# Kernel tuning notes

Hardware: AMD Instinct MI355X
Metric: run time of the kernel (lower is better)

## Reference

```python
import jax, jax.numpy as jnp
import numpy as np

EPS_CLAMP = 1.0 - 1e-06


def _patch_pool_view(x, H, W, p):
    # x: (n, H*W, s) with spatial flattened row-major over (H, W)
    # -> (n, (H//p)*(W//p), p*p, s), matching einops 'n (h ph w pw) s -> n (h w) (ph pw) s'
    n, q, s = x.shape
    h, w = H // p, W // p
    x = x.reshape(n, h, p, w, p, s)
    x = x.transpose(0, 1, 3, 2, 4, 5)  # n h w ph pw s
    return x.reshape(n, h * w, p * p, s)


def setup_inputs() -> dict:
    key = jax.random.key(0)
    k1, k2 = jax.random.split(key)
    N, C, H, W = 8, 256, 48, 48
    return {
        'mask_feats': jax.random.normal(k1, (N, C, H, W), dtype=jnp.float32),
        'query_feats_all': jax.random.normal(k2, (N, C, H, W), dtype=jnp.float32),
        'path_size': 4,
    }


def reference(mask_feats, query_feats_all, path_size):
    N, c_m, hm, wm = mask_feats.shape
    _, c_q, hq, wq = query_feats_all.shape
    # n c h w -> n (h w) c, scaled by 1/sqrt(c)
    mf = mask_feats.reshape(N, c_m, hm * wm).transpose(0, 2, 1) / (c_m ** 0.5)
    qf = query_feats_all.reshape(N, c_q, hq * wq).transpose(0, 2, 1) / (c_q ** 0.5)
    sim_matrix = jnp.einsum('nqc,nsc->nqs', qf, mf) * 10.0  # (N, Q, S)
    instance_masks = jax.nn.softmax(sim_matrix, axis=1)
    query_masks = jnp.swapaxes(jax.nn.softmax(sim_matrix, axis=2), 1, 2)  # (N, S, Q)
    # patch pooling (computed under torch.no_grad in original)
    tmp_instance_masks_d = jax.lax.stop_gradient(
        _patch_pool_view(instance_masks, hq, wq, path_size))
    instance_masks_d = jnp.minimum(tmp_instance_masks_d.sum(axis=2), EPS_CLAMP)
    tmp_query_masks_d = jax.lax.stop_gradient(
        _patch_pool_view(query_masks, hm, wm, path_size))
    query_masks_d = jnp.minimum(tmp_query_masks_d.sum(axis=2), EPS_CLAMP)
    return (instance_masks, query_masks, instance_masks_d, query_masks_d,
            tmp_instance_masks_d, tmp_query_masks_d)
```

## Files before the change

kernel.cpp:

```cpp
#include <hip/hip_runtime.h>
#include <hip/hip_bf16.h>

#define N_B 8
#define CH 256
#define HW 2304
#define SZ_QS (2304LL*2304LL)
#define SCALE 0.0390625f
#define EPSC 0.999999f

typedef __attribute__((ext_vector_type(8))) short bf8_t;
typedef __attribute__((ext_vector_type(4))) float f32x4;

#define O1 0LL
#define O2 42467328LL
#define O3 84934656LL
#define O4 87588864LL
#define O5 90243072LL
#define O6 132710400LL

__device__ __forceinline__ void gl_lds16(const unsigned short* g, unsigned short* l) {
  __builtin_amdgcn_global_load_lds(
      (const __attribute__((address_space(1))) unsigned int*)g,
      (__attribute__((address_space(3))) unsigned int*)l, 16, 0, 0);
}

__global__ __launch_bounds__(256) void k_tr(const float* __restrict__ q_in,
                                            const float* __restrict__ m_in,
                                            __hip_bfloat16* __restrict__ Abf,
                                            __hip_bfloat16* __restrict__ Bbf) {
  __shared__ float lds[64 * 65];
  const int n = blockIdx.z >> 1, which = blockIdx.z & 1;
  const float* src = which ? m_in : q_in;
  __hip_bfloat16* dst = which ? Bbf : Abf;
  const int q0 = blockIdx.x * 64, c0 = blockIdx.y * 64;
  const int tx = threadIdx.x & 63, ty = threadIdx.x >> 6;
#pragma unroll
  for (int p = 0; p < 16; ++p) {
    const int cl = p * 4 + ty;
    lds[cl * 65 + tx] = src[((size_t)n * CH + c0 + cl) * HW + q0 + tx];
  }
  __syncthreads();
#pragma unroll
  for (int p = 0; p < 16; ++p) {
    const int ql = p * 4 + ty;
    dst[((size_t)n * HW + q0 + ql) * CH + c0 + tx] = __float2bfloat16(lds[tx * 65 + ql]);
  }
}

__global__ __launch_bounds__(256) void k_zero(float* __restrict__ p) {
  const int i = (blockIdx.x * 256 + threadIdx.x) * 4;
  *(float4*)(p + i) = make_float4(0.f, 0.f, 0.f, 0.f);
}

__global__ __launch_bounds__(256) void k_inv(const float* __restrict__ s,
                                             float* __restrict__ inv) {
  const int i = blockIdx.x * 256 + threadIdx.x;
  inv[i] = 1.0f / s[i];
}

template <int FULL>
__global__ __launch_bounds__(512) void k_g192(
    const unsigned short* __restrict__ Abf, const unsigned short* __restrict__ Bbf,
    float* __restrict__ out1, float* __restrict__ out2, float* __restrict__ out3,
    float* __restrict__ out4, float* __restrict__ out5, float* __restrict__ out6,
    float* __restrict__ rowsum, float* __restrict__ colsum,
    const float* __restrict__ invr, const float* __restrict__ invc) {
  __shared__ char smem[49152];
  unsigned short* lA = (unsigned short*)smem;
  unsigned short* lB = (unsigned short*)(smem + 24576);

  const int n = blockIdx.z;
  const int S0 = blockIdx.x * 192, Q0 = blockIdx.y * 192;
  const int t = threadIdx.x, l = t & 63, w = t >> 6;
  const int wm = w >> 2, wn = w & 3;
  const int g = l >> 4, c = l & 15;

  f32x4 acc[6][3];
#pragma unroll
  for (int mi = 0; mi < 6; ++mi)
#pragma unroll
    for (int ni = 0; ni < 3; ++ni) {
      f32x4 z = {0.f, 0.f, 0.f, 0.f};
      acc[mi][ni] = z;
    }

  const int r0w = w * 24;
  const int lrow = l >> 3, lc8 = l & 7;
  const int scol = (lc8 ^ lrow) * 8;
  const unsigned short* gA = Abf + ((size_t)n * HW + Q0 + r0w + lrow) * CH + scol;
  const unsigned short* gB = Bbf + ((size_t)n * HW + S0 + r0w + lrow) * CH + scol;
  unsigned short* dA = lA + r0w * 64;
  unsigned short* dB = lB + r0w * 64;

  for (int kc = 0; kc < 4; ++kc) {
    const int k0 = kc * 64;
    gl_lds16(gA + k0, dA);
    gl_lds16(gA + k0 + 8 * CH, dA + 8 * 64);
    gl_lds16(gA + k0 + 16 * CH, dA + 16 * 64);
    gl_lds16(gB + k0, dB);
    gl_lds16(gB + k0 + 8 * CH, dB + 8 * 64);
    gl_lds16(gB + k0 + 16 * CH, dB + 16 * 64);
    __syncthreads();
#pragma unroll
    for (int ks = 0; ks < 2; ++ks) {
      const int kb = ks * 4 + g;
      bf8_t af[6], bf_[3];
#pragma unroll
      for (int mi = 0; mi < 6; ++mi) {
        const int r = wm * 96 + mi * 16 + c;
        af[mi] = *(const bf8_t*)(lA + r * 64 + ((kb ^ (c & 7)) * 8));
      }
#pragma unroll
      for (int ni = 0; ni < 3; ++ni) {
        const int r = wn * 48 + ni * 16 + c;
        bf_[ni] = *(const bf8_t*)(lB + r * 64 + ((kb ^ (c & 7)) * 8));
      }
#pragma unroll
      for (int mi = 0; mi < 6; ++mi)
#pragma unroll
        for (int ni = 0; ni < 3; ++ni)
          acc[mi][ni] = __builtin_amdgcn_mfma_f32_16x16x32_bf16(af[mi], bf_[ni], acc[mi][ni], 0, 0, 0);
    }
    __syncthreads();
  }

#pragma unroll
  for (int mi = 0; mi < 6; ++mi)
#pragma unroll
    for (int ni = 0; ni < 3; ++ni)
#pragma unroll
      for (int r = 0; r < 4; ++r)
        acc[mi][ni][r] = __expf(acc[mi][ni][r] * SCALE);

  if (!FULL) {
#pragma unroll
    for (int mi = 0; mi < 6; ++mi)
#pragma unroll
      for (int r = 0; r < 4; ++r) {
        float v = acc[mi][0][r] + acc[mi][1][r] + acc[mi][2][r];
        v += __shfl_xor(v, 1, 64);
        v += __shfl_xor(v, 2, 64);
        v += __shfl_xor(v, 4, 64);
        v += __shfl_xor(v, 8, 64);
        if (c == 0) atomicAdd(&rowsum[n * HW + Q0 + wm * 96 + mi * 16 + g * 4 + r], v);
      }
#pragma unroll
    for (int ni = 0; ni < 3; ++ni) {
      float v = 0.f;
#pragma unroll
      for (int mi = 0; mi < 6; ++mi)
#pragma unroll
        for (int r = 0; r < 4; ++r) v += acc[mi][ni][r];
      v += __shfl_xor(v, 16, 64);
      v += __shfl_xor(v, 32, 64);
      if (g == 0) atomicAdd(&colsum[n * HW + S0 + wn * 48 + ni * 16 + c], v);
    }
    return;
  }

  float icv[3];
#pragma unroll
  for (int ni = 0; ni < 3; ++ni) icv[ni] = invc[n * HW + S0 + wn * 48 + ni * 16 + c];

  float* fb = (float*)smem;
  const int hq = blockIdx.y, bx = blockIdx.x;

#pragma unroll
  for (int ch = 0; ch < 4; ++ch) {
    if (wm == (ch >> 1)) {
#pragma unroll
      for (int m3 = 0; m3 < 3; ++m3) {
        const int mi = (ch & 1) * 3 + m3;
        const int rowb = m3 * 16 + g * 4;
#pragma unroll
        for (int ni = 0; ni < 3; ++ni) {
          const int colb = wn * 48 + ni * 16 + c;
#pragma unroll
          for (int r = 0; r < 4; ++r)
            fb[(rowb + r) * 196 + colb] = acc[mi][ni][r] * icv[ni];
        }
      }
    }
    __syncthreads();
#pragma unroll
    for (int j = 0; j < 5; ++j) {
      const int idx = t + j * 512;
      if (idx < 2304) {
        const int row = idx / 48, col4 = idx % 48;
        const float4 v = *(const float4*)(fb + row * 196 + col4 * 4);
        *(float4*)(out1 + ((size_t)n * HW + Q0 + ch * 48 + row) * HW + S0 + col4 * 4) = v;
        const size_t r5 = ((size_t)n * 144 + hq * 12 + (row >> 2)) * 16 + ch * 4 + (row & 3);
        *(float4*)(out5 + r5 * HW + S0 + col4 * 4) = v;
      }
    }
    __syncthreads();
  }

#pragma unroll
  for (int ch = 0; ch < 4; ++ch) {
    if (wn == ch) {
#pragma unroll
      for (int mi = 0; mi < 6; ++mi) {
        const int colf = wm * 96 + mi * 16 + g * 4;
        const f32x4 irv = *(const f32x4*)(invr + n * HW + Q0 + colf);
#pragma unroll
        for (int ni = 0; ni < 3; ++ni) {
          const f32x4 pq = acc[mi][ni] * irv;
          *(f32x4*)(fb + (ni * 16 + c) * 196 + colf) = pq;
        }
      }
    }
    __syncthreads();
#pragma unroll
    for (int j = 0; j < 5; ++j) {
      const int idx = t + j * 512;
      if (idx < 2304) {
        const int row = idx / 48, col4 = idx % 48;
        const float4 v = *(const float4*)(fb + row * 196 + col4 * 4);
        *(float4*)(out2 + ((size_t)n * HW + S0 + ch * 48 + row) * HW + Q0 + col4 * 4) = v;
        const size_t r6 = ((size_t)n * 144 + bx * 12 + (row >> 2)) * 16 + ch * 4 + (row & 3);
        *(float4*)(out6 + r6 * HW + Q0 + col4 * 4) = v;
      }
    }
    __syncthreads();
  }

#pragma unroll
  for (int m3 = 0; m3 < 3; ++m3) {
    const int b = m3 * 4 + g;
#pragma unroll
    for (int ni = 0; ni < 3; ++ni) {
      const int sl = wn * 48 + ni * 16 + c;
      float p = 0.f;
#pragma unroll
      for (int r = 0; r < 4; ++r) p += acc[m3][ni][r] + acc[m3 + 3][ni][r];
      fb[(wm * 12 + b) * 196 + sl] = p * icv[ni];
    }
  }
  __syncthreads();
#pragma unroll
  for (int j = 0; j < 5; ++j) {
    const int idx = t + j * 512;
    if (idx < 2304) {
      const int b = idx / 192, sl = idx % 192;
      const float v = fb[b * 196 + sl] + fb[(12 + b) * 196 + sl];
      out3[((size_t)n * 144 + hq * 12 + b) * HW + S0 + sl] = fminf(v, EPSC);
    }
  }
  __syncthreads();

#pragma unroll
  for (int mi = 0; mi < 6; ++mi) {
    const int qloc = wm * 96 + mi * 16 + g * 4;
    const f32x4 irv = *(const f32x4*)(invr + n * HW + Q0 + qloc);
#pragma unroll
    for (int ni = 0; ni < 3; ++ni) {
      f32x4 pq = acc[mi][ni] * irv;
#pragma unroll
      for (int r = 0; r < 4; ++r) {
        pq[r] += __shfl_xor(pq[r], 1, 64);
        pq[r] += __shfl_xor(pq[r], 2, 64);
      }
      if ((c & 3) == 0) {
        const int pc = ni * 4 + (c >> 2);
        *(f32x4*)(fb + (wn * 12 + pc) * 196 + qloc) = pq;
      }
    }
  }
  __syncthreads();
#pragma unroll
  for (int j = 0; j < 5; ++j) {
    const int idx = t + j * 512;
    if (idx < 2304) {
      const int pc = idx / 192, q = idx % 192;
      const float v = fb[pc * 196 + q] + fb[(12 + pc) * 196 + q] +
                      fb[(24 + pc) * 196 + q] + fb[(36 + pc) * 196 + q];
      out4[((size_t)n * 144 + bx * 12 + pc) * HW + Q0 + q] = fminf(v, EPSC);
    }
  }
}

__global__ __launch_bounds__(256) void k_gemm_old(const unsigned short* __restrict__ Abf,
                                                  const unsigned short* __restrict__ Bbf,
                                                  float* __restrict__ out1,
                                                  float* __restrict__ rowsum,
                                                  float* __restrict__ colsum) {
  __shared__ unsigned short lA[128 * 64];
  __shared__ unsigned short lB[128 * 64];
  const int n = blockIdx.z;
  const int s0 = blockIdx.x * 128, q0 = blockIdx.y * 128;
  const int t = threadIdx.x, l = t & 63, w = t >> 6;
  const int wm = w >> 1, wn = w & 1;
  f32x4 acc[4][4];
#pragma unroll
  for (int mi = 0; mi < 4; ++mi)
#pragma unroll
    for (int ni = 0; ni < 4; ++ni) {
      f32x4 z = {0.f, 0.f, 0.f, 0.f};
      acc[mi][ni] = z;
    }
  const size_t baseA = ((size_t)n * HW + q0) * CH;
  const size_t baseB = ((size_t)n * HW + s0) * CH;
  const int jj = t & 7, rr = t >> 3;
  for (int kc = 0; kc < 4; ++kc) {
    const int k0 = kc * 64;
#pragma unroll
    for (int i = 0; i < 4; ++i) {
      const int r = i * 32 + rr;
      bf8_t va = *(const bf8_t*)(Abf + baseA + (size_t)r * CH + k0 + jj * 8);
      bf8_t vb = *(const bf8_t*)(Bbf + baseB + (size_t)r * CH + k0 + jj * 8);
      *(bf8_t*)(lA + r * 64 + ((jj ^ (r & 7)) * 8)) = va;
      *(bf8_t*)(lB + r * 64 + ((jj ^ (r & 7)) * 8)) = vb;
    }
    __syncthreads();
#pragma unroll
    for (int ks = 0; ks < 2; ++ks) {
      const int kb = ks * 4 + (l >> 4);
      bf8_t af[4], bfr[4];
#pragma unroll
      for (int mi = 0; mi < 4; ++mi) {
        const int r = wm * 64 + mi * 16 + (l & 15);
        af[mi] = *(const bf8_t*)(lA + r * 64 + ((kb ^ (r & 7)) * 8));
      }
#pragma unroll
      for (int ni = 0; ni < 4; ++ni) {
        const int r = wn * 64 + ni * 16 + (l & 15);
        bfr[ni] = *(const bf8_t*)(lB + r * 64 + ((kb ^ (r & 7)) * 8));
      }
#pragma unroll
      for (int mi = 0; mi < 4; ++mi)
#pragma unroll
        for (int ni = 0; ni < 4; ++ni)
          acc[mi][ni] = __builtin_amdgcn_mfma_f32_16x16x32_bf16(af[mi], bfr[ni], acc[mi][ni], 0, 0, 0);
    }
    __syncthreads();
  }
  float rp[4][4], cp[4];
#pragma unroll
  for (int mi = 0; mi < 4; ++mi)
#pragma unroll
    for (int r = 0; r < 4; ++r) rp[mi][r] = 0.f;
#pragma unroll
  for (int ni = 0; ni < 4; ++ni) cp[ni] = 0.f;
#pragma unroll
  for (int mi = 0; mi < 4; ++mi) {
    const int row = q0 + wm * 64 + mi * 16 + (l >> 4) * 4;
#pragma unroll
    for (int ni = 0; ni < 4; ++ni) {
      const int col = s0 + wn * 64 + ni * 16 + (l & 15);
      const size_t ob = ((size_t)n * HW + row) * HW + col;
#pragma unroll
      for (int r = 0; r < 4; ++r) {
        const float e = __expf(acc[mi][ni][r] * SCALE);
        out1[ob + (size_t)r * HW] = e;
        rp[mi][r] += e;
        cp[ni] += e;
      }
    }
  }
#pragma unroll
  for (int mi = 0; mi < 4; ++mi)
#pragma unroll
    for (int r = 0; r < 4; ++r) {
      float v = rp[mi][r];
      v += __shfl_xor(v, 1, 64);
      v += __shfl_xor(v, 2, 64);
      v += __shfl_xor(v, 4, 64);
      v += __shfl_xor(v, 8, 64);
      if ((l & 15) == 0)
        atomicAdd(&rowsum[n * HW + q0 + wm * 64 + mi * 16 + (l >> 4) * 4 + r], v);
    }
#pragma unroll
  for (int ni = 0; ni < 4; ++ni) {
    float v = cp[ni];
    v += __shfl_xor(v, 16, 64);
    v += __shfl_xor(v, 32, 64);
    if (l < 16) atomicAdd(&colsum[n * HW + s0 + wn * 64 + ni * 16 + l], v);
  }
}

__global__ __launch_bounds__(192) void k_main(float* __restrict__ out1,
                                              float* __restrict__ out2,
                                              float* __restrict__ out3,
                                              float* __restrict__ out5,
                                              float* __restrict__ out6,
                                              const float* __restrict__ invr,
                                              const float* __restrict__ invc) {
  __shared__ float ldsT[192 * 49];
  const int n = blockIdx.z, h = blockIdx.y, sb = blockIdx.x;
  const int S0 = sb * 192;
  const int t = threadIdx.x;
  const int sg = S0 + t;
  const float icv = invc[n * HW + sg];
  const float* invr_n = invr + n * HW;
  float* e_base = out1 + (size_t)n * SZ_QS;
  const int Q0 = h * 192;
  float acc[12];
#pragma unroll
  for (int i = 0; i < 12; ++i) acc[i] = 0.f;
  for (int ph = 0; ph < 4; ++ph) {
    const int qf0 = Q0 + ph * 48;
#pragma unroll
    for (int wi = 0; wi < 12; ++wi) {
#pragma unroll
      for (int pw = 0; pw < 4; ++pw) {
        const int col = wi * 4 + pw;
        const int q = qf0 + col;
        const size_t eoff = (size_t)q * HW + sg;
        const float e = e_base[eoff];
        const float pi = e * icv;
        e_base[eoff] = pi;
        out5[((size_t)((n * 144 + h * 12 + wi) * 16 + (ph * 4 + pw))) * HW + sg] = pi;
        acc[wi] += pi;
        ldsT[t * 49 + col] = e * invr_n[q];
      }
    }
    __syncthreads();
    const int u = t & 3, sB = t >> 2;
#pragma unroll
    for (int pass = 0; pass < 4; ++pass) {
      const int sl = pass * 48 + sB;
      const int sgl = S0 + sl;
      const int rs_ = sgl / 48, cs = sgl % 48;
      const int sp = (rs_ >> 2) * 12 + (cs >> 2);
      const int spp = (rs_ & 3) * 4 + (cs & 3);
      const size_t o2row = ((size_t)n * HW + sgl) * HW + qf0;
      const size_t o6row = (((size_t)n * 144 + sp) * 16 + spp) * HW + qf0;
#pragma unroll
      for (int k = 0; k < 3; ++k) {
        const int slot = u + k * 4;
        float4 v;
        v.x = ldsT[sl * 49 + slot * 4 + 0];
        v.y = ldsT[sl * 49 + slot * 4 + 1];
        v.z = ldsT[sl * 49 + slot * 4 + 2];
        v.w = ldsT[sl * 49 + slot * 4 + 3];
        *(float4*)(out2 + o2row + slot * 4) = v;
        *(float4*)(out6 + o6row + slot * 4) = v;
      }
    }
    __syncthreads();
  }
#pragma unroll
  for (int wi = 0; wi < 12; ++wi)
    out3[((size_t)(n * 144 + h * 12 + wi)) * HW + sg] = fminf(acc[wi], EPSC);
}

__global__ __launch_bounds__(256) void k_qd(const float* __restrict__ out6,
                                            float* __restrict__ out4) {
  const int n = blockIdx.y, sp = blockIdx.x;
  const float* b6 = out6 + (((size_t)n * 144 + sp) * 16) * HW;
  float* b4 = out4 + ((size_t)n * 144 + sp) * HW;
  for (int i = 0; i < 9; ++i) {
    const int qq = i * 256 + threadIdx.x;
    float s = 0.f;
#pragma unroll
    for (int spp = 0; spp < 16; ++spp) s += b6[(size_t)spp * HW + qq];
    b4[qq] = fminf(s, EPSC);
  }
}

extern "C" void kernel_launch(void* const* d_in, const int* in_sizes, int n_in,
                              void* d_out, int out_size, void* d_ws, size_t ws_size,
                              hipStream_t stream) {
  const float* mask_f = (const float*)d_in[0];
  const float* query_f = (const float*)d_in[1];
  float* out = (float*)d_out;
  float* out1 = out + O1;
  float* out2 = out + O2;
  float* out3 = out + O3;
  float* out4 = out + O4;
  float* out5 = out + O5;
  float* out6 = out + O6;

  const size_t abytes = (size_t)N_B * HW * CH * 2;
  const size_t sbytes = (size_t)N_B * HW * 4;
  const size_t need = 2 * abytes + 4 * sbytes;

  if (ws_size >= need) {
    char* base = (char*)d_ws;
    __hip_bfloat16* Abf = (__hip_bfloat16*)base;
    __hip_bfloat16* Bbf = (__hip_bfloat16*)(base + abytes);
    float* sums = (float*)(base + 2 * abytes);
    float* invs = (float*)(base + 2 * abytes + 2 * sbytes);
    float* rowsum = sums;
    float* colsum = sums + N_B * HW;
    float* invr = invs;
    float* invc = invs + N_B * HW;

    k_tr<<<dim3(36, 4, 16), 256, 0, stream>>>(query_f, mask_f, Abf, Bbf);
    k_zero<<<dim3(36), 256, 0, stream>>>(sums);
    k_g192<0><<<dim3(12, 12, 8), 512, 0, stream>>>(
        (const unsigned short*)Abf, (const unsigned short*)Bbf,
        nullptr, nullptr, nullptr, nullptr, nullptr, nullptr,
        rowsum, colsum, nullptr, nullptr);
    k_inv<<<dim3(144), 256, 0, stream>>>(sums, invs);
    k_g192<1><<<dim3(12, 12, 8), 512, 0, stream>>>(
        (const unsigned short*)Abf, (const unsigned short*)Bbf,
        out1, out2, out3, out4, out5, out6,
        nullptr, nullptr, invr, invc);
  } else {
    __hip_bfloat16* Abf = (__hip_bfloat16*)out4;
    __hip_bfloat16* Bbf = (__hip_bfloat16*)out3;
    float* sums = (float*)((char*)out4 + abytes);
    float* invs = sums + 2 * (N_B * HW);
    float* rowsum = sums;
    float* colsum = sums + N_B * HW;
    float* invr = invs;
    float* invc = invs + N_B * HW;

    k_tr<<<dim3(36, 4, 16), 256, 0, stream>>>(query_f, mask_f, Abf, Bbf);
    k_zero<<<dim3(36), 256, 0, stream>>>(sums);
    k_gemm_old<<<dim3(18, 18, 8), 256, 0, stream>>>(
        (const unsigned short*)Abf, (const unsigned short*)Bbf, out1, rowsum, colsum);
    k_inv<<<dim3(144), 256, 0, stream>>>(sums, invs);
    k_main<<<dim3(12, 12, 8), 192, 0, stream>>>(out1, out2, out3, out5, out6, invr, invc);
    k_qd<<<dim3(144, 8), 256, 0, stream>>>(out6, out4);
  }
}
```

Baseline: 243.2 us.

## Use 4-wave blocks with 96x96 warp tiles and flattened batch-interleaved grid

The 192x192 GEMM+softmax-epilogue kernel moves from 8 waves (each computing 96x48) to 4 waves (each computing 96x96), doubling per-wave accumulators and per-thread load and store work. The 3D grid becomes a 1D grid with the batch index in the low bits, so consecutive blocks belong to different batches. The epilogue staging and the patch reductions are reworked to fit the new wave layout, including a pre-add of column groups before the shuffle reduction. The aim is more MFMA work per LDS fragment read, but the larger register footprint (144 accumulator floats per thread) may lower occupancy or cause spills.

```diff
diff --git a/kernel.cpp b/kernel.cpp
--- a/kernel.cpp
+++ b/kernel.cpp
@@ -59,7 +59,7 @@
 }
 
 template <int FULL>
-__global__ __launch_bounds__(512) void k_g192(
+__global__ __launch_bounds__(256) void k_g192(
     const unsigned short* __restrict__ Abf, const unsigned short* __restrict__ Bbf,
     float* __restrict__ out1, float* __restrict__ out2, float* __restrict__ out3,
     float* __restrict__ out4, float* __restrict__ out5, float* __restrict__ out6,
@@ -69,22 +69,24 @@
   unsigned short* lA = (unsigned short*)smem;
   unsigned short* lB = (unsigned short*)(smem + 24576);
 
-  const int n = blockIdx.z;
-  const int S0 = blockIdx.x * 192, Q0 = blockIdx.y * 192;
+  const int bid = blockIdx.x;
+  const int n = bid & 7, tile = bid >> 3;
+  const int bx = tile % 12, hq = tile / 12;
+  const int S0 = bx * 192, Q0 = hq * 192;
   const int t = threadIdx.x, l = t & 63, w = t >> 6;
-  const int wm = w >> 2, wn = w & 3;
+  const int wm = w >> 1, wn = w & 1;
   const int g = l >> 4, c = l & 15;
 
-  f32x4 acc[6][3];
+  f32x4 acc[6][6];
 #pragma unroll
   for (int mi = 0; mi < 6; ++mi)
 #pragma unroll
-    for (int ni = 0; ni < 3; ++ni) {
+    for (int ni = 0; ni < 6; ++ni) {
       f32x4 z = {0.f, 0.f, 0.f, 0.f};
       acc[mi][ni] = z;
     }
 
-  const int r0w = w * 24;
+  const int r0w = w * 48;
   const int lrow = l >> 3, lc8 = l & 7;
   const int scol = (lc8 ^ lrow) * 8;
   const unsigned short* gA = Abf + ((size_t)n * HW + Q0 + r0w + lrow) * CH + scol;
@@ -94,31 +96,30 @@
 
   for (int kc = 0; kc < 4; ++kc) {
     const int k0 = kc * 64;
-    gl_lds16(gA + k0, dA);
-    gl_lds16(gA + k0 + 8 * CH, dA + 8 * 64);
-    gl_lds16(gA + k0 + 16 * CH, dA + 16 * 64);
-    gl_lds16(gB + k0, dB);
-    gl_lds16(gB + k0 + 8 * CH, dB + 8 * 64);
-    gl_lds16(gB + k0 + 16 * CH, dB + 16 * 64);
+#pragma unroll
+    for (int i = 0; i < 6; ++i) {
+      gl_lds16(gA + k0 + (size_t)(8 * i) * CH, dA + 8 * i * 64);
+      gl_lds16(gB + k0 + (size_t)(8 * i) * CH, dB + 8 * i * 64);
+    }
     __syncthreads();
 #pragma unroll
     for (int ks = 0; ks < 2; ++ks) {
       const int kb = ks * 4 + g;
-      bf8_t af[6], bf_[3];
+      bf8_t af[6], bf_[6];
 #pragma unroll
       for (int mi = 0; mi < 6; ++mi) {
         const int r = wm * 96 + mi * 16 + c;
         af[mi] = *(const bf8_t*)(lA + r * 64 + ((kb ^ (c & 7)) * 8));
       }
 #pragma unroll
-      for (int ni = 0; ni < 3; ++ni) {
-        const int r = wn * 48 + ni * 16 + c;
+      for (int ni = 0; ni < 6; ++ni) {
+        const int r = wn * 96 + ni * 16 + c;
         bf_[ni] = *(const bf8_t*)(lB + r * 64 + ((kb ^ (c & 7)) * 8));
       }
 #pragma unroll
       for (int mi = 0; mi < 6; ++mi)
 #pragma unroll
-        for (int ni = 0; ni < 3; ++ni)
+        for (int ni = 0; ni < 6; ++ni)
           acc[mi][ni] = __builtin_amdgcn_mfma_f32_16x16x32_bf16(af[mi], bf_[ni], acc[mi][ni], 0, 0, 0);
     }
     __syncthreads();
@@ -127,7 +128,7 @@
 #pragma unroll
   for (int mi = 0; mi < 6; ++mi)
 #pragma unroll
-    for (int ni = 0; ni < 3; ++ni)
+    for (int ni = 0; ni < 6; ++ni)
 #pragma unroll
       for (int r = 0; r < 4; ++r)
         acc[mi][ni][r] = __expf(acc[mi][ni][r] * SCALE);
@@ -137,7 +138,9 @@
     for (int mi = 0; mi < 6; ++mi)
 #pragma unroll
       for (int r = 0; r < 4; ++r) {
-        float v = acc[mi][0][r] + acc[mi][1][r] + acc[mi][2][r];
+        float v = 0.f;
+#pragma unroll
+        for (int ni = 0; ni < 6; ++ni) v += acc[mi][ni][r];
         v += __shfl_xor(v, 1, 64);
         v += __shfl_xor(v, 2, 64);
         v += __shfl_xor(v, 4, 64);
@@ -145,7 +148,7 @@
         if (c == 0) atomicAdd(&rowsum[n * HW + Q0 + wm * 96 + mi * 16 + g * 4 + r], v);
       }
 #pragma unroll
-    for (int ni = 0; ni < 3; ++ni) {
+    for (int ni = 0; ni < 6; ++ni) {
       float v = 0.f;
 #pragma unroll
       for (int mi = 0; mi < 6; ++mi)
@@ -153,17 +156,16 @@
         for (int r = 0; r < 4; ++r) v += acc[mi][ni][r];
       v += __shfl_xor(v, 16, 64);
       v += __shfl_xor(v, 32, 64);
-      if (g == 0) atomicAdd(&colsum[n * HW + S0 + wn * 48 + ni * 16 + c], v);
+      if (g == 0) atomicAdd(&colsum[n * HW + S0 + wn * 96 + ni * 16 + c], v);
     }
     return;
   }
 
-  float icv[3];
-#pragma unroll
-  for (int ni = 0; ni < 3; ++ni) icv[ni] = invc[n * HW + S0 + wn * 48 + ni * 16 + c];
+  float icv[6];
+#pragma unroll
+  for (int ni = 0; ni < 6; ++ni) icv[ni] = invc[n * HW + S0 + wn * 96 + ni * 16 + c];
 
   float* fb = (float*)smem;
-  const int hq = blockIdx.y, bx = blockIdx.x;
 
 #pragma unroll
   for (int ch = 0; ch < 4; ++ch) {
@@ -173,8 +175,8 @@
         const int mi = (ch & 1) * 3 + m3;
         const int rowb = m3 * 16 + g * 4;
 #pragma unroll
-        for (int ni = 0; ni < 3; ++ni) {
-          const int colb = wn * 48 + ni * 16 + c;
+        for (int ni = 0; ni < 6; ++ni) {
+          const int colb = wn * 96 + ni * 16 + c;
 #pragma unroll
           for (int r = 0; r < 4; ++r)
             fb[(rowb + r) * 196 + colb] = acc[mi][ni][r] * icv[ni];
@@ -183,44 +185,42 @@
     }
     __syncthreads();
 #pragma unroll
-    for (int j = 0; j < 5; ++j) {
-      const int idx = t + j * 512;
-      if (idx < 2304) {
-        const int row = idx / 48, col4 = idx % 48;
-        const float4 v = *(const float4*)(fb + row * 196 + col4 * 4);
-        *(float4*)(out1 + ((size_t)n * HW + Q0 + ch * 48 + row) * HW + S0 + col4 * 4) = v;
-        const size_t r5 = ((size_t)n * 144 + hq * 12 + (row >> 2)) * 16 + ch * 4 + (row & 3);
-        *(float4*)(out5 + r5 * HW + S0 + col4 * 4) = v;
-      }
+    for (int j = 0; j < 9; ++j) {
+      const int idx = t + j * 256;
+      const int row = idx / 48, col4 = idx % 48;
+      const float4 v = *(const float4*)(fb + row * 196 + col4 * 4);
+      *(float4*)(out1 + ((size_t)n * HW + Q0 + ch * 48 + row) * HW + S0 + col4 * 4) = v;
+      const size_t r5 = ((size_t)n * 144 + hq * 12 + (row >> 2)) * 16 + ch * 4 + (row & 3);
+      *(float4*)(out5 + r5 * HW + S0 + col4 * 4) = v;
     }
     __syncthreads();
   }
 
 #pragma unroll
   for (int ch = 0; ch < 4; ++ch) {
-    if (wn == ch) {
-#pragma unroll
-      for (int mi = 0; mi < 6; ++mi) {
-        const int colf = wm * 96 + mi * 16 + g * 4;
-        const f32x4 irv = *(const f32x4*)(invr + n * HW + Q0 + colf);
-#pragma unroll
-        for (int ni = 0; ni < 3; ++ni) {
+    if (wn == (ch >> 1)) {
+#pragma unroll
+      for (int n3 = 0; n3 < 3; ++n3) {
+        const int ni = (ch & 1) * 3 + n3;
+        const int rowb = n3 * 16 + c;
+#pragma unroll
+        for (int mi = 0; mi < 6; ++mi) {
+          const int colf = wm * 96 + mi * 16 + g * 4;
+          const f32x4 irv = *(const f32x4*)(invr + n * HW + Q0 + colf);
           const f32x4 pq = acc[mi][ni] * irv;
-          *(f32x4*)(fb + (ni * 16 + c) * 196 + colf) = pq;
+          *(f32x4*)(fb + rowb * 196 + colf) = pq;
         }
       }
     }
     __syncthreads();
 #pragma unroll
-    for (int j = 0; j < 5; ++j) {
-      const int idx = t + j * 512;
-      if (idx < 2304) {
-        const int row = idx / 48, col4 = idx % 48;
-        const float4 v = *(const float4*)(fb + row * 196 + col4 * 4);
-        *(float4*)(out2 + ((size_t)n * HW + S0 + ch * 48 + row) * HW + Q0 + col4 * 4) = v;
-        const size_t r6 = ((size_t)n * 144 + bx * 12 + (row >> 2)) * 16 + ch * 4 + (row & 3);
-        *(float4*)(out6 + r6 * HW + Q0 + col4 * 4) = v;
-      }
+    for (int j = 0; j < 9; ++j) {
+      const int idx = t + j * 256;
+      const int row = idx / 48, col4 = idx % 48;
+      const float4 v = *(const float4*)(fb + row * 196 + col4 * 4);
+      *(float4*)(out2 + ((size_t)n * HW + S0 + ch * 48 + row) * HW + Q0 + col4 * 4) = v;
+      const size_t r6 = ((size_t)n * 144 + bx * 12 + (row >> 2)) * 16 + ch * 4 + (row & 3);
+      *(float4*)(out6 + r6 * HW + Q0 + col4 * 4) = v;
     }
     __syncthreads();
   }
@@ -229,8 +229,8 @@
   for (int m3 = 0; m3 < 3; ++m3) {
     const int b = m3 * 4 + g;
 #pragma unroll
-    for (int ni = 0; ni < 3; ++ni) {
-      const int sl = wn * 48 + ni * 16 + c;
+    for (int ni = 0; ni < 6; ++ni) {
+      const int sl = wn * 96 + ni * 16 + c;
       float p = 0.f;
 #pragma unroll
       for (int r = 0; r < 4; ++r) p += acc[m3][ni][r] + acc[m3 + 3][ni][r];
@@ -239,13 +239,11 @@
   }
   __syncthreads();
 #pragma unroll
-  for (int j = 0; j < 5; ++j) {
-    const int idx = t + j * 512;
-    if (idx < 2304) {
-      const int b = idx / 192, sl = idx % 192;
-      const float v = fb[b * 196 + sl] + fb[(12 + b) * 196 + sl];
-      out3[((size_t)n * 144 + hq * 12 + b) * HW + S0 + sl] = fminf(v, EPSC);
-    }
+  for (int j = 0; j < 9; ++j) {
+    const int idx = t + j * 256;
+    const int b = idx / 192, sl = idx % 192;
+    const float v = fb[b * 196 + sl] + fb[(12 + b) * 196 + sl];
+    out3[((size_t)n * 144 + hq * 12 + b) * HW + S0 + sl] = fminf(v, EPSC);
   }
   __syncthreads();
 
@@ -254,29 +252,26 @@
     const int qloc = wm * 96 + mi * 16 + g * 4;
     const f32x4 irv = *(const f32x4*)(invr + n * HW + Q0 + qloc);
 #pragma unroll
-    for (int ni = 0; ni < 3; ++ni) {
-      f32x4 pq = acc[mi][ni] * irv;
+    for (int n3 = 0; n3 < 3; ++n3) {
+      f32x4 v = (acc[mi][n3] + acc[mi][n3 + 3]) * irv;
 #pragma unroll
       for (int r = 0; r < 4; ++r) {
-        pq[r] += __shfl_xor(pq[r], 1, 64);
-        pq[r] += __shfl_xor(pq[r], 2, 64);
+        v[r] += __shfl_xor(v[r], 1, 64);
+        v[r] += __shfl_xor(v[r], 2, 64);
       }
       if ((c & 3) == 0) {
-        const int pc = ni * 4 + (c >> 2);
-        *(f32x4*)(fb + (wn * 12 + pc) * 196 + qloc) = pq;
+        const int pc = n3 * 4 + (c >> 2);
+        *(f32x4*)(fb + (wn * 12 + pc) * 196 + qloc) = v;
       }
     }
   }
   __syncthreads();
 #pragma unroll
-  for (int j = 0; j < 5; ++j) {
-    const int idx = t + j * 512;
-    if (idx < 2304) {
-      const int pc = idx / 192, q = idx % 192;
-      const float v = fb[pc * 196 + q] + fb[(12 + pc) * 196 + q] +
-                      fb[(24 + pc) * 196 + q] + fb[(36 + pc) * 196 + q];
-      out4[((size_t)n * 144 + bx * 12 + pc) * HW + Q0 + q] = fminf(v, EPSC);
-    }
+  for (int j = 0; j < 9; ++j) {
+    const int idx = t + j * 256;
+    const int pc = idx / 192, q = idx % 192;
+    const float v = fb[pc * 196 + q] + fb[(12 + pc) * 196 + q];
+    out4[((size_t)n * 144 + bx * 12 + pc) * HW + Q0 + q] = fminf(v, EPSC);
   }
 }
 
@@ -489,12 +484,12 @@
 
     k_tr<<<dim3(36, 4, 16), 256, 0, stream>>>(query_f, mask_f, Abf, Bbf);
     k_zero<<<dim3(36), 256, 0, stream>>>(sums);
-    k_g192<0><<<dim3(12, 12, 8), 512, 0, stream>>>(
+    k_g192<0><<<dim3(1152), 256, 0, stream>>>(
         (const unsigned short*)Abf, (const unsigned short*)Bbf,
         nullptr, nullptr, nullptr, nullptr, nullptr, nullptr,
         rowsum, colsum, nullptr, nullptr);
     k_inv<<<dim3(144), 256, 0, stream>>>(sums, invs);
-    k_g192<1><<<dim3(12, 12, 8), 512, 0, stream>>>(
+    k_g192<1><<<dim3(1152), 256, 0, stream>>>(
         (const unsigned short*)Abf, (const unsigned short*)Bbf,
         out1, out2, out3, out4, out5, out6,
         nullptr, nullptr, invr, invc);
```

Result: slower. 249.7 us, median of 2 (+2.7%).
